# Kernel tuning notes

Hardware: AMD Instinct MI355X
Metric: run time of the kernel (lower is better)

## Reference

```python
import jax, jax.numpy as jnp
import numpy as np

N_NODES = 100000
N_EDGES = 1600000
F_IN = 64
HIDDEN = 64
N_CLASSES = 2


def setup_inputs() -> dict:
    key = jax.random.key(0)
    k1, k2, k3, k4, k5, k6 = jax.random.split(key, 6)
    x = jax.random.normal(k1, (N_NODES, F_IN), dtype=jnp.float32)
    edge_index = jax.random.randint(k2, (2, N_EDGES), 0, N_NODES, dtype=jnp.int64)
    # Glorot-ish init for GCNConv linear weights, zero bias (PyG default)
    W1 = jax.random.normal(k3, (F_IN, HIDDEN), dtype=jnp.float32) * (1.0 / np.sqrt(F_IN))
    b1 = jnp.zeros((HIDDEN,), dtype=jnp.float32)
    W2 = jax.random.normal(k4, (HIDDEN, N_CLASSES), dtype=jnp.float32) * (1.0 / np.sqrt(HIDDEN))
    b2 = jnp.zeros((N_CLASSES,), dtype=jnp.float32)
    return {"x": x, "edge_index": edge_index, "W1": W1, "b1": b1, "W2": W2, "b2": b2}


def _gcn_norm(edge_index, num_nodes):
    # Add self-loops, then symmetric normalization D^-1/2 (A+I) D^-1/2
    loops = jnp.arange(num_nodes, dtype=edge_index.dtype)
    row = jnp.concatenate([edge_index[0], loops])  # [E+N] targets
    col = jnp.concatenate([edge_index[1], loops])  # [E+N] sources
    deg = jax.ops.segment_sum(jnp.ones(row.shape[0], jnp.float32), row, num_segments=num_nodes)
    dinv = jnp.where(deg > 0, jax.lax.rsqrt(deg), 0.0)
    norm = dinv[row] * dinv[col]  # [E+N]
    return row, col, norm


def _gcn_conv(x, W, b, row, col, norm, num_nodes):
    h = x @ W                                   # [N, out]
    msg = h[col] * norm[:, None]                # gather + scale, [E+N, out]
    agg = jax.ops.segment_sum(msg, row, num_segments=num_nodes)  # scatter-add
    return agg + b


def reference(x, edge_index, W1, b1, W2, b2):
    n = x.shape[0]
    row, col, norm = _gcn_norm(edge_index, n)
    h = jax.nn.relu(_gcn_conv(x, W1, b1, row, col, norm, n))
    # dropout p=0.5 is identity in eval mode
    logits = _gcn_conv(h, W2, b2, row, col, norm, n)
    return jax.nn.softmax(logits, axis=1)
```

## Files before the change

### kernel.cpp

```cpp
#include <hip/hip_runtime.h>
#include <hip/hip_fp16.h>


#define NBKT(n) (((n) + 255) >> 8)

__global__ __launch_bounds__(256) void k_bucketcount(const int* __restrict__ row,
                                                     int* __restrict__ bcnt,
                                                     __half* __restrict__ hp,
                                                     int E, int nb, int N) {
    __shared__ int cnt[392];
    int tid = threadIdx.x;
    int base = blockIdx.x * 4096;
    int m = E - base; if (m > 4096) m = 4096;
    for (int t = tid; t < nb; t += 256) cnt[t] = 0;
    __syncthreads();
    for (int i = tid; i < m; i += 256) atomicAdd(&cnt[row[base + i] >> 8], 1);
    __syncthreads();
    for (int t = tid; t < nb; t += 256) {
        int v = cnt[t];
        if (v > 0) atomicAdd(&bcnt[t], v);
    }
    if (blockIdx.x == 0 && tid < 32) ((int*)(hp + (size_t)N * 64))[tid] = 0;
}

__global__ __launch_bounds__(256) void k_bin(const int* __restrict__ row,
                                             const int* __restrict__ col,
                                             const int* __restrict__ bcnt,
                                             int* __restrict__ relcur,
                                             unsigned* __restrict__ pairbuf,
                                             int E, int nb) {
    __shared__ unsigned items[4096];
    __shared__ unsigned short bktid[4096];
    __shared__ int cnt[392];
    __shared__ int start0[392];
    __shared__ int cursor[392];
    __shared__ int gb[392];
    __shared__ int gbase[392];

    int tid = threadIdx.x;
    int base = blockIdx.x * 4096;
    int m = E - base; if (m > 4096) m = 4096;

    for (int t = tid; t < nb; t += 256) cnt[t] = 0;
    __syncthreads();
    for (int i = tid; i < m; i += 256) atomicAdd(&cnt[row[base + i] >> 8], 1);
    __syncthreads();
    if (tid < 64) {
        int lane = tid, running = 0;
        for (int ch = 0; ch < 7; ++ch) {
            int idx = ch * 64 + lane;
            int v = (idx < nb) ? cnt[idx] : 0;
            int s = v;
#pragma unroll
            for (int off = 1; off < 64; off <<= 1) {
                int t = __shfl_up(s, off, 64);
                if (lane >= off) s += t;
            }
            if (idx < nb) { start0[idx] = running + s - v; cursor[idx] = running + s - v; }
            running += __shfl(s, 63, 64);
        }
    } else if (tid < 128) {
        int lane = tid - 64, running = 0;
        for (int ch = 0; ch < 7; ++ch) {
            int idx = ch * 64 + lane;
            int v = (idx < nb) ? bcnt[idx] : 0;
            int s = v;
#pragma unroll
            for (int off = 1; off < 64; off <<= 1) {
                int t = __shfl_up(s, off, 64);
                if (lane >= off) s += t;
            }
            if (idx < nb) gb[idx] = running + s - v;
            running += __shfl(s, 63, 64);
        }
    }
    __syncthreads();
    for (int i = tid; i < m; i += 256) {
        int r = row[base + i];
        int c = col[base + i];
        int b = r >> 8;
        int pos = atomicAdd(&cursor[b], 1);
        items[pos] = ((unsigned)(r & 255) << 24) | (unsigned)c;
        bktid[pos] = (unsigned short)b;
    }
    __syncthreads();
    for (int t = tid; t < nb; t += 256) {
        int cv = cnt[t];
        if (cv > 0) gbase[t] = gb[t] + atomicAdd(&relcur[t], cv);
    }
    __syncthreads();
    for (int i = tid; i < m; i += 256) {
        int b = bktid[i];
        pairbuf[gbase[b] + (i - start0[b])] = items[i];
    }
}

__global__ __launch_bounds__(256) void k_sortnode(const unsigned* __restrict__ pairbuf,
                                                  const int* __restrict__ bcnt,
                                                  int* __restrict__ scol,
                                                  int* __restrict__ offsets,
                                                  float* __restrict__ dinv,
                                                  int N, int E) {
    __shared__ int ps[256];
    __shared__ int cnt[256];
    __shared__ int tmp[256];
    __shared__ int cur[256];
    int b = blockIdx.x;
    int tid = threadIdx.x;
    int v = (tid < b) ? bcnt[tid] : 0;
    if (tid + 256 < b) v += bcnt[tid + 256];
    ps[tid] = v;
    __syncthreads();
    for (int s = 128; s >= 1; s >>= 1) {
        if (tid < s) ps[tid] += ps[tid + s];
        __syncthreads();
    }
    int lo = ps[0];
    int hi = lo + bcnt[b];
    cnt[tid] = 0;
    __syncthreads();
    for (int i = lo + tid; i < hi; i += 256)
        atomicAdd(&cnt[pairbuf[i] >> 24], 1);
    __syncthreads();
    int cv = cnt[tid];
    tmp[tid] = cv;
    __syncthreads();
    for (int d = 1; d < 256; d <<= 1) {
        int t = (tid >= (unsigned)d) ? tmp[tid - d] : 0;
        __syncthreads();
        if (tid >= (unsigned)d) tmp[tid] += t;
        __syncthreads();
    }
    int excl = tmp[tid] - cv;
    int n = (b << 8) + tid;
    if (n < N) {
        offsets[n] = lo + excl;
        dinv[n] = rsqrtf((float)(cv + 1));
    }
    cur[tid] = lo + excl;
    if (b == 0 && tid == 0) { offsets[N] = E; scol[E] = N; }
    __syncthreads();
    for (int i = lo + tid; i < hi; i += 256) {
        unsigned it = pairbuf[i];
        int pos = atomicAdd(&cur[it >> 24], 1);
        scol[pos] = (int)(it & 0xFFFFFFu);
    }
}

__global__ __launch_bounds__(256, 1) void k_gemm1(const float* __restrict__ x,
                                                  const float* __restrict__ W1,
                                                  const float* __restrict__ dinv,
                                                  __half* __restrict__ hp, int N) {
    int lane = threadIdx.x & 63;
    float w1c[64];
#pragma unroll
    for (int k = 0; k < 64; ++k) w1c[k] = W1[k * 64 + lane];
    int wv = (int)((blockIdx.x * 256 + threadIdx.x) >> 6);
    int nw = (int)((gridDim.x * 256) >> 6);
    for (int n = wv; n < N; n += nw) {
        int nu = __builtin_amdgcn_readfirstlane(n);
        const float* xr = x + (size_t)nu * 64;
        float a0 = 0.f, a1 = 0.f, a2 = 0.f, a3 = 0.f;
#pragma unroll
        for (int k = 0; k < 64; k += 4) {
            a0 = fmaf(xr[k + 0], w1c[k + 0], a0);
            a1 = fmaf(xr[k + 1], w1c[k + 1], a1);
            a2 = fmaf(xr[k + 2], w1c[k + 2], a2);
            a3 = fmaf(xr[k + 3], w1c[k + 3], a3);
        }
        float acc = (a0 + a1) + (a2 + a3);
        hp[(size_t)nu * 64 + lane] = __float2half(dinv[nu] * acc);
    }
}

__global__ __launch_bounds__(256) void k_agg1(const __half* __restrict__ hp,
                                              const int* __restrict__ offsets,
                                              const int* __restrict__ sorted_col,
                                              const float* __restrict__ dinv,
                                              const float* __restrict__ b1,
                                              const float* __restrict__ W2,
                                              float2* __restrict__ h2p, int N, int E) {
    int lane = threadIdx.x & 63;
    int slot = lane >> 3;
    int chunk = lane & 7;
    int wid = (int)((blockIdx.x * 256 + threadIdx.x) >> 6);
    int n = wid * 8 + slot;
    int nc = (n < N) ? n : N;
    int start = offsets[nc];
    int end = offsets[(n < N) ? (n + 1) : N];
    int deg = end - start;
    int maxd = deg;
#pragma unroll
    for (int s = 8; s <= 32; s <<= 1) {
        int o = __shfl_xor(maxd, s, 64);
        maxd = (o > maxd) ? o : maxd;
    }
    const float4* hp4 = (const float4*)hp;
    float4 sr = hp4[(size_t)nc * 8 + chunk];
    __half2 acc0 = ((const __half2*)&sr)[0];
    __half2 acc1 = ((const __half2*)&sr)[1];
    __half2 acc2 = ((const __half2*)&sr)[2];
    __half2 acc3 = ((const __half2*)&sr)[3];
    for (int j0 = 0; j0 < maxd; j0 += 4) {
        int a0 = (j0 + 0 < deg) ? (start + j0 + 0) : E;
        int a1 = (j0 + 1 < deg) ? (start + j0 + 1) : E;
        int a2 = (j0 + 2 < deg) ? (start + j0 + 2) : E;
        int a3 = (j0 + 3 < deg) ? (start + j0 + 3) : E;
        int c0 = sorted_col[a0];
        int c1 = sorted_col[a1];
        int c2 = sorted_col[a2];
        int c3 = sorted_col[a3];
        float4 r0 = hp4[(size_t)c0 * 8 + chunk];
        float4 r1 = hp4[(size_t)c1 * 8 + chunk];
        float4 r2 = hp4[(size_t)c2 * 8 + chunk];
        float4 r3 = hp4[(size_t)c3 * 8 + chunk];
        const __half2* h0 = (const __half2*)&r0;
        const __half2* h1_ = (const __half2*)&r1;
        const __half2* h2_ = (const __half2*)&r2;
        const __half2* h3 = (const __half2*)&r3;
        acc0 = __hadd2(acc0, h0[0]); acc1 = __hadd2(acc1, h0[1]);
        acc2 = __hadd2(acc2, h0[2]); acc3 = __hadd2(acc3, h0[3]);
        acc0 = __hadd2(acc0, h1_[0]); acc1 = __hadd2(acc1, h1_[1]);
        acc2 = __hadd2(acc2, h1_[2]); acc3 = __hadd2(acc3, h1_[3]);
        acc0 = __hadd2(acc0, h2_[0]); acc1 = __hadd2(acc1, h2_[1]);
        acc2 = __hadd2(acc2, h2_[2]); acc3 = __hadd2(acc3, h2_[3]);
        acc0 = __hadd2(acc0, h3[0]); acc1 = __hadd2(acc1, h3[1]);
        acc2 = __hadd2(acc2, h3[2]); acc3 = __hadd2(acc3, h3[3]);
    }
    float af[8];
    { float2 f;
      f = __half22float2(acc0); af[0] = f.x; af[1] = f.y;
      f = __half22float2(acc1); af[2] = f.x; af[3] = f.y;
      f = __half22float2(acc2); af[4] = f.x; af[5] = f.y;
      f = __half22float2(acc3); af[6] = f.x; af[7] = f.y; }
    float dn = dinv[(n < N) ? n : (N - 1)];
    float4 b1a = ((const float4*)b1)[chunk * 2];
    float4 b1b = ((const float4*)b1)[chunk * 2 + 1];
    float h1[8];
    h1[0] = fmaxf(fmaf(dn, af[0], b1a.x), 0.f);
    h1[1] = fmaxf(fmaf(dn, af[1], b1a.y), 0.f);
    h1[2] = fmaxf(fmaf(dn, af[2], b1a.z), 0.f);
    h1[3] = fmaxf(fmaf(dn, af[3], b1a.w), 0.f);
    h1[4] = fmaxf(fmaf(dn, af[4], b1b.x), 0.f);
    h1[5] = fmaxf(fmaf(dn, af[5], b1b.y), 0.f);
    h1[6] = fmaxf(fmaf(dn, af[6], b1b.z), 0.f);
    h1[7] = fmaxf(fmaf(dn, af[7], b1b.w), 0.f);
    float p0 = 0.f, p1 = 0.f;
#pragma unroll
    for (int k = 0; k < 4; ++k) {
        float4 w = ((const float4*)W2)[chunk * 4 + k];
        p0 = fmaf(h1[2 * k], w.x, p0); p1 = fmaf(h1[2 * k], w.y, p1);
        p0 = fmaf(h1[2 * k + 1], w.z, p0); p1 = fmaf(h1[2 * k + 1], w.w, p1);
    }
#pragma unroll
    for (int s = 1; s <= 4; s <<= 1) {
        p0 += __shfl_xor(p0, s, 64);
        p1 += __shfl_xor(p1, s, 64);
    }
    if (chunk == 0 && n < N) h2p[n] = make_float2(dn * p0, dn * p1);
}

__global__ __launch_bounds__(256) void k_agg2(const float2* __restrict__ h2p,
                                              const int* __restrict__ offsets,
                                              const int* __restrict__ sorted_col,
                                              const float* __restrict__ dinv,
                                              const float* __restrict__ b2,
                                              float2* __restrict__ out, int N) {
    int gtid = blockIdx.x * 256 + threadIdx.x;
    int n = gtid >> 4;
    int sub = threadIdx.x & 15;
    if (n >= N) return;
    int start = offsets[n], end = offsets[n + 1];
    float ax = 0.f, ay = 0.f;
    if (sub == 0) { float2 s = h2p[n]; ax = s.x; ay = s.y; }
    for (int j = start + sub; j < end; j += 16) {
        float2 v = h2p[sorted_col[j]];
        ax += v.x; ay += v.y;
    }
#pragma unroll
    for (int s = 1; s <= 8; s <<= 1) {
        ax += __shfl_xor(ax, s, 64);
        ay += __shfl_xor(ay, s, 64);
    }
    if (sub == 0) {
        float dn = dinv[n];
        float l0 = fmaf(dn, ax, b2[0]), l1 = fmaf(dn, ay, b2[1]);
        float m = fmaxf(l0, l1);
        float e0 = __expf(l0 - m), e1 = __expf(l1 - m);
        float inv = 1.0f / (e0 + e1);
        out[n] = make_float2(e0 * inv, e1 * inv);
    }
}

extern "C" void kernel_launch(void* const* d_in, const int* in_sizes, int n_in,
                              void* d_out, int out_size, void* d_ws, size_t ws_size,
                              hipStream_t stream) {
    const float* x  = (const float*)d_in[0];
    const int*   ei = (const int*)d_in[1];
    const float* W1 = (const float*)d_in[2];
    const float* b1 = (const float*)d_in[3];
    const float* W2 = (const float*)d_in[4];
    const float* b2 = (const float*)d_in[5];
    float2* out = (float2*)d_out;

    const int N = in_sizes[0] / 64;
    const int E = in_sizes[1] / 2;
    const int nb = NBKT(N);
    const int* row = ei;
    const int* col = ei + E;

    char* p = (char*)d_ws;
    auto alloc = [&](size_t bytes) -> void* {
        void* r = (void*)p;
        p += (bytes + 255) & ~(size_t)255;
        return r;
    };
    int*   bcnt    = (int*)alloc(784 * 4);
    int*   relcur  = bcnt + 392;
    int*   offsets = (int*)alloc((size_t)(N + 1) * 4);
    float* dinv    = (float*)alloc((size_t)N * 4);
    unsigned* pairbuf = (unsigned*)alloc((size_t)E * 4);
    int*   scol    = (int*)alloc((size_t)(E + 1) * 4);
    __half* hp     = (__half*)alloc((size_t)(N + 1) * 64 * 2);
    float2* h2p    = (float2*)alloc((size_t)N * 8);

    const int nTile = (E + 4095) / 4096;

    hipMemsetAsync(bcnt, 0, 784 * 4, stream);
    k_bucketcount<<<nTile, 256, 0, stream>>>(row, bcnt, hp, E, nb, N);
    k_bin<<<nTile, 256, 0, stream>>>(row, col, bcnt, relcur, pairbuf, E, nb);
    k_sortnode<<<nb, 256, 0, stream>>>(pairbuf, bcnt, scol, offsets, dinv, N, E);
    k_gemm1<<<2048, 256, 0, stream>>>(x, W1, dinv, hp, N);
    const int nwaves = (N + 7) / 8;
    k_agg1<<<(nwaves + 3) / 4, 256, 0, stream>>>(hp, offsets, scol, dinv, b1, W2, h2p, N, E);
    k_agg2<<<(N * 16 + 255) / 256, 256, 0, stream>>>(h2p, offsets, scol, dinv, b2, out, N);
}
```

Baseline: 200.4 us.

## Compute first-layer GEMM with fp16 MFMA 16x16x32 tiles

Replaces the per-row scalar FMA loop in k_gemm1 with MFMA f16 matrix instructions. Each wave now processes 16-row tiles, loads x with float4 vector loads and converts them to fp16, and keeps W1 in fp16 register fragments. The grid shrinks from 2048 to 512 blocks and launch bounds allow two blocks per CU. Converting x and W1 to fp16 before the multiply reduces precision. Rows beyond the last multiple of 16 (N>>4 tiles) are not handled, which is only correct because N=100000 is divisible by 16.

```diff
diff --git a/kernel.cpp b/kernel.cpp
--- a/kernel.cpp
+++ b/kernel.cpp
@@ -3,6 +3,9 @@
 
 
 #define NBKT(n) (((n) + 255) >> 8)
+
+typedef _Float16 f16x8 __attribute__((ext_vector_type(8)));
+typedef float f32x4 __attribute__((ext_vector_type(4)));
 
 __global__ __launch_bounds__(256) void k_bucketcount(const int* __restrict__ row,
                                                      int* __restrict__ bcnt,
@@ -147,29 +150,54 @@
     }
 }
 
-__global__ __launch_bounds__(256, 1) void k_gemm1(const float* __restrict__ x,
+__global__ __launch_bounds__(256, 2) void k_gemm1(const float* __restrict__ x,
                                                   const float* __restrict__ W1,
                                                   const float* __restrict__ dinv,
                                                   __half* __restrict__ hp, int N) {
     int lane = threadIdx.x & 63;
-    float w1c[64];
-#pragma unroll
-    for (int k = 0; k < 64; ++k) w1c[k] = W1[k * 64 + lane];
+    int q = lane >> 4;
+    int m = lane & 15;
+    f16x8 bf[4][2];
+#pragma unroll
+    for (int nt = 0; nt < 4; ++nt)
+#pragma unroll
+        for (int kk = 0; kk < 2; ++kk)
+#pragma unroll
+            for (int j = 0; j < 8; ++j)
+                bf[nt][kk][j] = (_Float16)W1[(kk * 32 + q * 8 + j) * 64 + nt * 16 + m];
     int wv = (int)((blockIdx.x * 256 + threadIdx.x) >> 6);
     int nw = (int)((gridDim.x * 256) >> 6);
-    for (int n = wv; n < N; n += nw) {
-        int nu = __builtin_amdgcn_readfirstlane(n);
-        const float* xr = x + (size_t)nu * 64;
-        float a0 = 0.f, a1 = 0.f, a2 = 0.f, a3 = 0.f;
-#pragma unroll
-        for (int k = 0; k < 64; k += 4) {
-            a0 = fmaf(xr[k + 0], w1c[k + 0], a0);
-            a1 = fmaf(xr[k + 1], w1c[k + 1], a1);
-            a2 = fmaf(xr[k + 2], w1c[k + 2], a2);
-            a3 = fmaf(xr[k + 3], w1c[k + 3], a3);
+    int T = N >> 4;
+    for (int t = wv; t < T; t += nw) {
+        const float* xrow = x + (size_t)(t * 16 + m) * 64;
+        float4 u0 = *(const float4*)(xrow + q * 8);
+        float4 u1 = *(const float4*)(xrow + q * 8 + 4);
+        float4 u2 = *(const float4*)(xrow + 32 + q * 8);
+        float4 u3 = *(const float4*)(xrow + 32 + q * 8 + 4);
+        f16x8 a0, a1;
+        a0[0] = (_Float16)u0.x; a0[1] = (_Float16)u0.y; a0[2] = (_Float16)u0.z; a0[3] = (_Float16)u0.w;
+        a0[4] = (_Float16)u1.x; a0[5] = (_Float16)u1.y; a0[6] = (_Float16)u1.z; a0[7] = (_Float16)u1.w;
+        a1[0] = (_Float16)u2.x; a1[1] = (_Float16)u2.y; a1[2] = (_Float16)u2.z; a1[3] = (_Float16)u2.w;
+        a1[4] = (_Float16)u3.x; a1[5] = (_Float16)u3.y; a1[6] = (_Float16)u3.z; a1[7] = (_Float16)u3.w;
+        f32x4 ac0 = {0.f, 0.f, 0.f, 0.f}, ac1 = ac0, ac2 = ac0, ac3 = ac0;
+        ac0 = __builtin_amdgcn_mfma_f32_16x16x32_f16(a0, bf[0][0], ac0, 0, 0, 0);
+        ac1 = __builtin_amdgcn_mfma_f32_16x16x32_f16(a0, bf[1][0], ac1, 0, 0, 0);
+        ac2 = __builtin_amdgcn_mfma_f32_16x16x32_f16(a0, bf[2][0], ac2, 0, 0, 0);
+        ac3 = __builtin_amdgcn_mfma_f32_16x16x32_f16(a0, bf[3][0], ac3, 0, 0, 0);
+        ac0 = __builtin_amdgcn_mfma_f32_16x16x32_f16(a1, bf[0][1], ac0, 0, 0, 0);
+        ac1 = __builtin_amdgcn_mfma_f32_16x16x32_f16(a1, bf[1][1], ac1, 0, 0, 0);
+        ac2 = __builtin_amdgcn_mfma_f32_16x16x32_f16(a1, bf[2][1], ac2, 0, 0, 0);
+        ac3 = __builtin_amdgcn_mfma_f32_16x16x32_f16(a1, bf[3][1], ac3, 0, 0, 0);
+#pragma unroll
+        for (int reg = 0; reg < 4; ++reg) {
+            int rr = t * 16 + q * 4 + reg;
+            float dv = dinv[rr];
+            __half* dst = hp + (size_t)rr * 64 + m;
+            dst[0]  = __float2half(dv * ac0[reg]);
+            dst[16] = __float2half(dv * ac1[reg]);
+            dst[32] = __float2half(dv * ac2[reg]);
+            dst[48] = __float2half(dv * ac3[reg]);
         }
-        float acc = (a0 + a1) + (a2 + a3);
-        hp[(size_t)nu * 64 + lane] = __float2half(dinv[nu] * acc);
     }
 }
 
@@ -330,7 +358,7 @@
     k_bucketcount<<<nTile, 256, 0, stream>>>(row, bcnt, hp, E, nb, N);
     k_bin<<<nTile, 256, 0, stream>>>(row, col, bcnt, relcur, pairbuf, E, nb);
     k_sortnode<<<nb, 256, 0, stream>>>(pairbuf, bcnt, scol, offsets, dinv, N, E);
-    k_gemm1<<<2048, 256, 0, stream>>>(x, W1, dinv, hp, N);
+    k_gemm1<<<512, 256, 0, stream>>>(x, W1, dinv, hp, N);
     const int nwaves = (N + 7) / 8;
     k_agg1<<<(nwaves + 3) / 4, 256, 0, stream>>>(hp, offsets, scol, dinv, b1, W2, h2p, N, E);
     k_agg2<<<(N * 16 + 255) / 256, 256, 0, stream>>>(h2p, offsets, scol, dinv, b2, out, N);
```

New measurement: 181.8 us. 9.3% less time.
